# Performance work log

Hardware: AMD Instinct MI355X
Metric: run time of the kernel (lower is better)

## Reference

```python
import jax, jax.numpy as jnp
import numpy as np

ALPHA = 0.2  # LeakyReLU negative slope
NEG_BIG = -9e15


def setup_inputs() -> dict:
    key = jax.random.key(0)
    k1, k2, k3, k4 = jax.random.split(key, 4)
    N, F_IN, F_OUT = 8192, 256, 128
    h = jax.random.normal(k1, (N, F_IN), dtype=jnp.float32)
    adj = jax.random.randint(k2, (N, N), 0, 2, dtype=jnp.int32)
    # xavier_uniform with gain=1.414
    def xavier(k, shape, gain=1.414):
        fan_in, fan_out = shape[0], shape[1]
        bound = gain * np.sqrt(6.0 / (fan_in + fan_out))
        return jax.random.uniform(k, shape, jnp.float32, -bound, bound)
    W = xavier(k3, (F_IN, F_OUT))
    a = xavier(k4, (2 * F_OUT, 1))
    return {"h": h, "adj": adj, "W": W, "a": a}


def reference(h, adj, W, a):
    # Wh: [N, F_out]
    Wh = h @ W
    F_out = W.shape[1]
    a1 = a[:F_out, 0]   # attends to source (row) node
    a2 = a[F_out:, 0]   # attends to target (col) node
    # Additive decomposition of concat([Wh_i, Wh_j]) @ a:
    # e[i, j] = leaky_relu(Wh_i . a1 + Wh_j . a2)
    f1 = Wh @ a1  # [N]
    f2 = Wh @ a2  # [N]
    e = jax.nn.leaky_relu(f1[:, None] + f2[None, :], negative_slope=ALPHA)  # [N, N]
    scores = jnp.where(adj > 0, e, jnp.float32(NEG_BIG))
    attention = jax.nn.softmax(scores, axis=1)
    # dropout is identity in eval mode (training=False)
    h_prime = attention @ Wh  # [N, F_out]
    return h_prime
```

## Files before the change

kernel.cpp:

```cpp
#include <hip/hip_runtime.h>


#define N_NODES 8192
#define F_IN 256
#define F_OUT 128
#define RPB 32
#define JCH 128
#define JSPLIT 2
#define JRANGE (N_NODES / JSPLIT)
#define NCH (JRANGE / JCH)

typedef _Float16 half8 __attribute__((ext_vector_type(8)));
typedef float floatx4 __attribute__((ext_vector_type(4)));
typedef float f32x4 __attribute__((ext_vector_type(4)));

__device__ __align__(16) float g_Wh[N_NODES * F_OUT];
__device__ __align__(16) _Float16 g_WhT[(size_t)F_OUT * N_NODES];
__device__ __align__(16) float g_f1[N_NODES];
__device__ __align__(16) float g_f2[N_NODES];
__device__ __align__(16) float g_part[JSPLIT][N_NODES * F_OUT];
__device__ __align__(16) float g_spart[JSPLIT][N_NODES];

__global__ __launch_bounds__(256, 2) void wh_kernel(
    const float* __restrict__ h, const float* __restrict__ W) {
  __shared__ float hT[F_IN][20];
  const int t = threadIdx.x;
  const int i0 = blockIdx.x * 16;
  {
    const int row = t >> 4;
    const int fu = t & 15;
#pragma unroll
    for (int r = 0; r < 4; ++r) {
      const int ku = r * 16 + fu;
      const float4 v = *(const float4*)(h + (size_t)(i0 + row) * F_IN + ku * 4);
      hT[ku * 4 + 0][row] = v.x; hT[ku * 4 + 1][row] = v.y;
      hT[ku * 4 + 2][row] = v.z; hT[ku * 4 + 3][row] = v.w;
    }
  }
  __syncthreads();
  const int c = t & 127;
  const int rg = t >> 7;
  float acc[8];
#pragma unroll
  for (int r = 0; r < 8; ++r) acc[r] = 0.f;
#pragma unroll 8
  for (int k = 0; k < F_IN; ++k) {
    const float wv = W[k * F_OUT + c];
    const float4 x0 = *(const float4*)(&hT[k][rg * 8]);
    const float4 x1 = *(const float4*)(&hT[k][rg * 8 + 4]);
    acc[0] = fmaf(x0.x, wv, acc[0]); acc[1] = fmaf(x0.y, wv, acc[1]);
    acc[2] = fmaf(x0.z, wv, acc[2]); acc[3] = fmaf(x0.w, wv, acc[3]);
    acc[4] = fmaf(x1.x, wv, acc[4]); acc[5] = fmaf(x1.y, wv, acc[5]);
    acc[6] = fmaf(x1.z, wv, acc[6]); acc[7] = fmaf(x1.w, wv, acc[7]);
  }
#pragma unroll
  for (int r = 0; r < 8; ++r)
    g_Wh[(size_t)(i0 + rg * 8 + r) * F_OUT + c] = acc[r];
  union { _Float16 hh[8]; uint4 u4; } pk;
#pragma unroll
  for (int r = 0; r < 8; ++r) pk.hh[r] = (_Float16)acc[r];
  *(uint4*)(g_WhT + (size_t)c * N_NODES + i0 + rg * 8) = pk.u4;
}

__global__ __launch_bounds__(256) void f12_kernel(const float* __restrict__ a) {
  const int t = threadIdx.x;
  const int row = blockIdx.x * 2 + (t >> 7);
  const int c = t & 127;
  const float wh = g_Wh[(size_t)row * F_OUT + c];
  float p1 = wh * a[c];
  float p2 = wh * a[F_OUT + c];
  for (int o = 32; o > 0; o >>= 1) {
    p1 += __shfl_down(p1, o, 64);
    p2 += __shfl_down(p2, o, 64);
  }
  __shared__ float s1[4], s2[4];
  const int w = t >> 6;
  if ((t & 63) == 0) { s1[w] = p1; s2[w] = p2; }
  __syncthreads();
  if ((t & 127) == 0) {
    g_f1[row] = s1[w] + s1[w + 1];
    g_f2[row] = s2[w] + s2[w + 1];
  }
}

__device__ __forceinline__ float score_p(int a, float f2v, float f1r) {
  float s = f1r + f2v;
  s = fmaxf(s, 0.2f * s);
  float arg = (a > 0) ? fmaf(s, 1.44269504088896f, -16.0f) : -1.0e5f;
  return __builtin_amdgcn_exp2f(arg);
}

__global__ __launch_bounds__(256, 2) void gat_attn_kernel(const int* __restrict__ adj) {
  const int t = threadIdx.x;
  const int wave = t >> 6;
  const int lane = t & 63;
  const int mrow = lane & 15;
  const int quad = lane >> 4;
  const int i0 = blockIdx.x * RPB;
  const int js = blockIdx.y;
  const int jbase = js * JRANGE;

  __shared__ float ldsF2[JRANGE];
  __shared__ float ldsO[RPB][F_OUT];
  __shared__ float ldsS[4][RPB];

  int rm[4], cm[4];
  {
    half8 a1f, b1f, a2f, b2f;
#pragma unroll
    for (int e = 0; e < 8; ++e) {
      a1f[e] = (_Float16)0; b1f[e] = (_Float16)0;
      a2f[e] = (_Float16)0; b2f[e] = (_Float16)0;
    }
    if (quad == 0) {
      a1f[0] = (_Float16)mrow; b1f[0] = (_Float16)1;
      a2f[0] = (_Float16)1;    b2f[0] = (_Float16)mrow;
    }
    floatx4 d1 = (floatx4)0.f, d2 = (floatx4)0.f;
    d1 = __builtin_amdgcn_mfma_f32_16x16x32_f16(a1f, b1f, d1, 0, 0, 0);
    d2 = __builtin_amdgcn_mfma_f32_16x16x32_f16(a2f, b2f, d2, 0, 0, 0);
#pragma unroll
    for (int r = 0; r < 4; ++r) { rm[r] = (int)d1[r]; cm[r] = (int)d2[r]; }
  }

  const float f1r0 = g_f1[i0 + mrow];
  const float f1r1 = g_f1[i0 + 16 + mrow];

  half8 ones;
#pragma unroll
  for (int e = 0; e < 8; ++e) ones[e] = (_Float16)1;

  floatx4 acc[2][8];
  floatx4 asum[2];
#pragma unroll
  for (int tl = 0; tl < 2; ++tl) {
    asum[tl] = (floatx4)0.f;
#pragma unroll
    for (int ct = 0; ct < 8; ++ct) acc[tl][ct] = (floatx4)0.f;
  }

#pragma unroll
  for (int it = 0; it < 4; ++it) {
    const int u = it * 256 + t;
    *(float4*)&ldsF2[u * 4] = *(const float4*)(g_f2 + jbase + u * 4);
  }
  __syncthreads();

  const size_t rowoff0 = (size_t)(i0 + mrow) * N_NODES;
  const size_t rowoff1 = (size_t)(i0 + 16 + mrow) * N_NODES;
  const int jloc = wave * 32 + quad * 8;

#pragma unroll 1
  for (int c = 0; c < NCH; ++c) {
    const int jglob = jbase + c * JCH + jloc;

    const int4 A00 = *(const int4*)(adj + rowoff0 + jglob);
    const int4 A01 = *(const int4*)(adj + rowoff0 + jglob + 4);
    const int4 A10 = *(const int4*)(adj + rowoff1 + jglob);
    const int4 A11 = *(const int4*)(adj + rowoff1 + jglob + 4);

    half8 bfr[8];
#pragma unroll
    for (int ct = 0; ct < 8; ++ct)
      bfr[ct] = *(const half8*)(g_WhT + (size_t)(ct * 16 + mrow) * N_NODES + jglob);

    const float4 F0 = *(const float4*)&ldsF2[c * JCH + jloc];
    const float4 F1 = *(const float4*)&ldsF2[c * JCH + jloc + 4];

    half8 af0, af1;
    af0[0] = (_Float16)score_p(A00.x, F0.x, f1r0);
    af0[1] = (_Float16)score_p(A00.y, F0.y, f1r0);
    af0[2] = (_Float16)score_p(A00.z, F0.z, f1r0);
    af0[3] = (_Float16)score_p(A00.w, F0.w, f1r0);
    af0[4] = (_Float16)score_p(A01.x, F1.x, f1r0);
    af0[5] = (_Float16)score_p(A01.y, F1.y, f1r0);
    af0[6] = (_Float16)score_p(A01.z, F1.z, f1r0);
    af0[7] = (_Float16)score_p(A01.w, F1.w, f1r0);
    af1[0] = (_Float16)score_p(A10.x, F0.x, f1r1);
    af1[1] = (_Float16)score_p(A10.y, F0.y, f1r1);
    af1[2] = (_Float16)score_p(A10.z, F0.z, f1r1);
    af1[3] = (_Float16)score_p(A10.w, F0.w, f1r1);
    af1[4] = (_Float16)score_p(A11.x, F1.x, f1r1);
    af1[5] = (_Float16)score_p(A11.y, F1.y, f1r1);
    af1[6] = (_Float16)score_p(A11.z, F1.z, f1r1);
    af1[7] = (_Float16)score_p(A11.w, F1.w, f1r1);

#pragma unroll
    for (int ct = 0; ct < 8; ++ct) {
      acc[0][ct] = __builtin_amdgcn_mfma_f32_16x16x32_f16(af0, bfr[ct], acc[0][ct], 0, 0, 0);
      acc[1][ct] = __builtin_amdgcn_mfma_f32_16x16x32_f16(af1, bfr[ct], acc[1][ct], 0, 0, 0);
    }
    asum[0] = __builtin_amdgcn_mfma_f32_16x16x32_f16(af0, ones, asum[0], 0, 0, 0);
    asum[1] = __builtin_amdgcn_mfma_f32_16x16x32_f16(af1, ones, asum[1], 0, 0, 0);
  }

  if (mrow == 0) {
#pragma unroll
    for (int tl = 0; tl < 2; ++tl)
#pragma unroll
      for (int r = 0; r < 4; ++r)
        ldsS[wave][tl * 16 + rm[r]] = asum[tl][r];
  }
  for (int w = 0; w < 4; ++w) {
    if (wave == w) {
#pragma unroll
      for (int tl = 0; tl < 2; ++tl)
#pragma unroll
        for (int ct = 0; ct < 8; ++ct)
#pragma unroll
          for (int r = 0; r < 4; ++r) {
            float* p = &ldsO[tl * 16 + rm[r]][ct * 16 + cm[r]];
            if (w == 0) *p = acc[tl][ct][r];
            else        *p += acc[tl][ct][r];
          }
    }
    __syncthreads();
  }
  {
    const int row = t >> 3;
    const int c0 = (t & 7) * 16;
    float* dst = g_part[js] + (size_t)(i0 + row) * F_OUT + c0;
#pragma unroll
    for (int q = 0; q < 4; ++q)
      *(f32x4*)(dst + q * 4) = *(const f32x4*)(&ldsO[row][c0 + q * 4]);
    if (t < RPB)
      g_spart[js][i0 + t] = ldsS[0][t] + ldsS[1][t] + ldsS[2][t] + ldsS[3][t];
  }
}

__global__ __launch_bounds__(256) void comb_kernel(float* __restrict__ out) {
  const int u = blockIdx.x * 256 + threadIdx.x;
  const int row = u >> 5;
  const float s = g_spart[0][row] + g_spart[1][row];
  const f32x4 v = ((const f32x4*)g_part[0])[u] + ((const f32x4*)g_part[1])[u];
  ((f32x4*)out)[u] = v * (1.0f / s);
}

extern "C" void kernel_launch(void* const* d_in, const int* in_sizes, int n_in,
                              void* d_out, int out_size, void* d_ws, size_t ws_size,
                              hipStream_t stream) {
  const float* h = (const float*)d_in[0];
  const int* adj = (const int*)d_in[1];
  const float* W = (const float*)d_in[2];
  const float* a = (const float*)d_in[3];
  float* out = (float*)d_out;
  (void)d_ws; (void)ws_size;

  wh_kernel<<<dim3(N_NODES / 16), dim3(256), 0, stream>>>(h, W);
  f12_kernel<<<dim3(N_NODES / 2), dim3(256), 0, stream>>>(a);
  gat_attn_kernel<<<dim3(N_NODES / RPB, JSPLIT), dim3(256), 0, stream>>>(adj);
  comb_kernel<<<dim3(N_NODES * F_OUT / 4 / 256), dim3(256), 0, stream>>>(out);
}
```

Measured before the change: 451.7 us.

## Pre-pack adjacency into bitmask and read bits in attention kernel

Adds a pre-pass kernel that compresses the int32 adjacency matrix into a swizzled bitmask laid out for the attention kernel's lane mapping. The attention kernel then loads one dword per four chunks instead of 32 bytes of int adjacency per chunk, which removes heavy global loads from the MFMA loop, and it raises the occupancy hint to three blocks. The full adjacency read still happens in the new pass, plus an extra launch and an 8 MB intermediate write/read.

```diff
diff --git a/kernel.cpp b/kernel.cpp
--- a/kernel.cpp
+++ b/kernel.cpp
@@ -20,6 +20,37 @@
 __device__ __align__(16) float g_f2[N_NODES];
 __device__ __align__(16) float g_part[JSPLIT][N_NODES * F_OUT];
 __device__ __align__(16) float g_spart[JSPLIT][N_NODES];
+__device__ __align__(16) unsigned char g_bits[(size_t)N_NODES * (N_NODES / 8)];
+
+__global__ __launch_bounds__(256) void pack_kernel(const int* __restrict__ adj) {
+  const int t = threadIdx.x;
+  const int wave = t >> 6;
+  const int lane = t & 63;
+  const int row0 = blockIdx.x * 8 + wave * 2;
+#pragma unroll 1
+  for (int rr = 0; rr < 2; ++rr) {
+    const int r = row0 + rr;
+    const int* rowp = adj + (size_t)r * N_NODES;
+#pragma unroll 4
+    for (int p = 0; p < 16; ++p) {
+      const int j0 = p * 512 + lane * 8;
+      const int4 v0 = *(const int4*)(rowp + j0);
+      const int4 v1 = *(const int4*)(rowp + j0 + 4);
+      unsigned int byte = 0;
+      byte |= (v0.x != 0) ? 1u : 0u;
+      byte |= (v0.y != 0) ? 2u : 0u;
+      byte |= (v0.z != 0) ? 4u : 0u;
+      byte |= (v0.w != 0) ? 8u : 0u;
+      byte |= (v1.x != 0) ? 16u : 0u;
+      byte |= (v1.y != 0) ? 32u : 0u;
+      byte |= (v1.z != 0) ? 64u : 0u;
+      byte |= (v1.w != 0) ? 128u : 0u;
+      const int b = p * 64 + lane;
+      const int addr = r * 1024 + (((b >> 2) & 3) * 4 + (b & 3)) * 64 + (b >> 4);
+      g_bits[addr] = (unsigned char)byte;
+    }
+  }
+}
 
 __global__ __launch_bounds__(256, 2) void wh_kernel(
     const float* __restrict__ h, const float* __restrict__ W) {
@@ -83,14 +114,14 @@
   }
 }
 
-__device__ __forceinline__ float score_p(int a, float f2v, float f1r) {
+__device__ __forceinline__ float score_b(unsigned int bit, float f2v, float f1r) {
   float s = f1r + f2v;
   s = fmaxf(s, 0.2f * s);
-  float arg = (a > 0) ? fmaf(s, 1.44269504088896f, -16.0f) : -1.0e5f;
+  float arg = bit ? fmaf(s, 1.44269504088896f, -16.0f) : -1.0e5f;
   return __builtin_amdgcn_exp2f(arg);
 }
 
-__global__ __launch_bounds__(256, 2) void gat_attn_kernel(const int* __restrict__ adj) {
+__global__ __launch_bounds__(256, 3) void gat_attn_kernel() {
   const int t = threadIdx.x;
   const int wave = t >> 6;
   const int lane = t & 63;
@@ -146,52 +177,57 @@
   }
   __syncthreads();
 
-  const size_t rowoff0 = (size_t)(i0 + mrow) * N_NODES;
-  const size_t rowoff1 = (size_t)(i0 + 16 + mrow) * N_NODES;
+  const int wq = wave * 4 + quad;
   const int jloc = wave * 32 + quad * 8;
+  const unsigned char* bp0 = g_bits + (i0 + mrow) * 1024 + wq * 64 + js * 32;
+  const unsigned char* bp1 = g_bits + (i0 + 16 + mrow) * 1024 + wq * 64 + js * 32;
 
 #pragma unroll 1
-  for (int c = 0; c < NCH; ++c) {
-    const int jglob = jbase + c * JCH + jloc;
-
-    const int4 A00 = *(const int4*)(adj + rowoff0 + jglob);
-    const int4 A01 = *(const int4*)(adj + rowoff0 + jglob + 4);
-    const int4 A10 = *(const int4*)(adj + rowoff1 + jglob);
-    const int4 A11 = *(const int4*)(adj + rowoff1 + jglob + 4);
-
-    half8 bfr[8];
-#pragma unroll
-    for (int ct = 0; ct < 8; ++ct)
-      bfr[ct] = *(const half8*)(g_WhT + (size_t)(ct * 16 + mrow) * N_NODES + jglob);
-
-    const float4 F0 = *(const float4*)&ldsF2[c * JCH + jloc];
-    const float4 F1 = *(const float4*)&ldsF2[c * JCH + jloc + 4];
-
-    half8 af0, af1;
-    af0[0] = (_Float16)score_p(A00.x, F0.x, f1r0);
-    af0[1] = (_Float16)score_p(A00.y, F0.y, f1r0);
-    af0[2] = (_Float16)score_p(A00.z, F0.z, f1r0);
-    af0[3] = (_Float16)score_p(A00.w, F0.w, f1r0);
-    af0[4] = (_Float16)score_p(A01.x, F1.x, f1r0);
-    af0[5] = (_Float16)score_p(A01.y, F1.y, f1r0);
-    af0[6] = (_Float16)score_p(A01.z, F1.z, f1r0);
-    af0[7] = (_Float16)score_p(A01.w, F1.w, f1r0);
-    af1[0] = (_Float16)score_p(A10.x, F0.x, f1r1);
-    af1[1] = (_Float16)score_p(A10.y, F0.y, f1r1);
-    af1[2] = (_Float16)score_p(A10.z, F0.z, f1r1);
-    af1[3] = (_Float16)score_p(A10.w, F0.w, f1r1);
-    af1[4] = (_Float16)score_p(A11.x, F1.x, f1r1);
-    af1[5] = (_Float16)score_p(A11.y, F1.y, f1r1);
-    af1[6] = (_Float16)score_p(A11.z, F1.z, f1r1);
-    af1[7] = (_Float16)score_p(A11.w, F1.w, f1r1);
-
-#pragma unroll
-    for (int ct = 0; ct < 8; ++ct) {
-      acc[0][ct] = __builtin_amdgcn_mfma_f32_16x16x32_f16(af0, bfr[ct], acc[0][ct], 0, 0, 0);
-      acc[1][ct] = __builtin_amdgcn_mfma_f32_16x16x32_f16(af1, bfr[ct], acc[1][ct], 0, 0, 0);
-    }
-    asum[0] = __builtin_amdgcn_mfma_f32_16x16x32_f16(af0, ones, asum[0], 0, 0, 0);
-    asum[1] = __builtin_amdgcn_mfma_f32_16x16x32_f16(af1, ones, asum[1], 0, 0, 0);
+  for (int c4 = 0; c4 < NCH / 4; ++c4) {
+    const unsigned int dw0 = *(const unsigned int*)(bp0 + c4 * 4);
+    const unsigned int dw1 = *(const unsigned int*)(bp1 + c4 * 4);
+#pragma unroll
+    for (int k = 0; k < 4; ++k) {
+      const int c = c4 * 4 + k;
+      const int jglob = jbase + c * JCH + jloc;
+
+      half8 bfr[8];
+#pragma unroll
+      for (int ct = 0; ct < 8; ++ct)
+        bfr[ct] = *(const half8*)(g_WhT + (size_t)(ct * 16 + mrow) * N_NODES + jglob);
+
+      const float4 F0 = *(const float4*)&ldsF2[c * JCH + jloc];
+      const float4 F1 = *(const float4*)&ldsF2[c * JCH + jloc + 4];
+
+      const unsigned int b0 = (dw0 >> (8 * k)) & 0xffu;
+      const unsigned int b1 = (dw1 >> (8 * k)) & 0xffu;
+
+      half8 af0, af1;
+      af0[0] = (_Float16)score_b(b0 & 1u,   F0.x, f1r0);
+      af0[1] = (_Float16)score_b(b0 & 2u,   F0.y, f1r0);
+      af0[2] = (_Float16)score_b(b0 & 4u,   F0.z, f1r0);
+      af0[3] = (_Float16)score_b(b0 & 8u,   F0.w, f1r0);
+      af0[4] = (_Float16)score_b(b0 & 16u,  F1.x, f1r0);
+      af0[5] = (_Float16)score_b(b0 & 32u,  F1.y, f1r0);
+      af0[6] = (_Float16)score_b(b0 & 64u,  F1.z, f1r0);
+      af0[7] = (_Float16)score_b(b0 & 128u, F1.w, f1r0);
+      af1[0] = (_Float16)score_b(b1 & 1u,   F0.x, f1r1);
+      af1[1] = (_Float16)score_b(b1 & 2u,   F0.y, f1r1);
+      af1[2] = (_Float16)score_b(b1 & 4u,   F0.z, f1r1);
+      af1[3] = (_Float16)score_b(b1 & 8u,   F0.w, f1r1);
+      af1[4] = (_Float16)score_b(b1 & 16u,  F1.x, f1r1);
+      af1[5] = (_Float16)score_b(b1 & 32u,  F1.y, f1r1);
+      af1[6] = (_Float16)score_b(b1 & 64u,  F1.z, f1r1);
+      af1[7] = (_Float16)score_b(b1 & 128u, F1.w, f1r1);
+
+#pragma unroll
+      for (int ct = 0; ct < 8; ++ct) {
+        acc[0][ct] = __builtin_amdgcn_mfma_f32_16x16x32_f16(af0, bfr[ct], acc[0][ct], 0, 0, 0);
+        acc[1][ct] = __builtin_amdgcn_mfma_f32_16x16x32_f16(af1, bfr[ct], acc[1][ct], 0, 0, 0);
+      }
+      asum[0] = __builtin_amdgcn_mfma_f32_16x16x32_f16(af0, ones, asum[0], 0, 0, 0);
+      asum[1] = __builtin_amdgcn_mfma_f32_16x16x32_f16(af1, ones, asum[1], 0, 0, 0);
+    }
   }
 
   if (mrow == 0) {
@@ -246,8 +282,9 @@
   float* out = (float*)d_out;
   (void)d_ws; (void)ws_size;
 
+  pack_kernel<<<dim3(N_NODES / 8), dim3(256), 0, stream>>>(adj);
   wh_kernel<<<dim3(N_NODES / 16), dim3(256), 0, stream>>>(h, W);
   f12_kernel<<<dim3(N_NODES / 2), dim3(256), 0, stream>>>(a);
-  gat_attn_kernel<<<dim3(N_NODES / RPB, JSPLIT), dim3(256), 0, stream>>>(adj);
+  gat_attn_kernel<<<dim3(N_NODES / RPB, JSPLIT), dim3(256), 0, stream>>>();
   comb_kernel<<<dim3(N_NODES * F_OUT / 4 / 256), dim3(256), 0, stream>>>(out);
 }
```

After: 472.1 us. +4.5%, slower.
